# Kernel optimization log

Hardware: AMD Instinct MI355X
Metric: run time of the kernel (lower is better)

## Reference

```python
import jax, jax.numpy as jnp
import numpy as np

NEG_SLOPE = 0.2
EPS = 1e-16


def gat_layer(x, src, dst, W, att, bias, heads, out_ch, concat, num_nodes, edge_weight):
    """WeightedGATConv forward (eval mode, dropout off).
    x: [N, Fin], src/dst: [E], W: [Fin, H*C], att: [H, 2C], bias: [H*C] or [C].
    """
    H, C = heads, out_ch
    xp = (x @ W).reshape(-1, H, C)           # [N, H, C]
    xi = xp[dst]                              # target features  [E, H, C]
    xj = xp[src]                              # source features  [E, H, C]
    # attention logits: (cat(xi, xj) * att).sum(-1)
    alpha = jnp.einsum('ehc,hc->eh', xi, att[:, :C]) + jnp.einsum('ehc,hc->eh', xj, att[:, C:])
    alpha = jnp.where(alpha >= 0, alpha, NEG_SLOPE * alpha)   # leaky_relu
    # segment softmax over incoming edges of each destination node
    amax = jax.ops.segment_max(alpha, dst, num_segments=num_nodes)  # [N, H]
    amax = jnp.where(jnp.isfinite(amax), amax, 0.0)
    ex = jnp.exp(alpha - amax[dst])                                  # [E, H]
    denom = jax.ops.segment_sum(ex, dst, num_segments=num_nodes)     # [N, H]
    a = ex / (denom[dst] + EPS)                                      # [E, H]
    msg = xj * a[..., None]                                          # [E, H, C]
    if edge_weight is not None:
        msg = msg * edge_weight[:, None, None]
    out = jax.ops.segment_sum(msg, dst, num_segments=num_nodes)      # [N, H, C]
    out = out.reshape(num_nodes, H * C) if concat else out.mean(axis=1)
    return out + bias


def setup_inputs() -> dict:
    key = jax.random.key(0)
    ks = jax.random.split(key, 10)
    N, E = 20000, 320000
    IN, HID, LAT, H = 512, 256, 128, 4
    C1 = HID // H
    glorot = lambda k, shp: jax.random.uniform(k, shp, jnp.float32, -1.0, 1.0) * jnp.sqrt(6.0 / (shp[-2] + shp[-1]))
    return {
        'x': jax.random.normal(ks[0], (N, IN), jnp.float32),
        'edge_index': jax.random.randint(ks[1], (2, E), 0, N, jnp.int32),
        'edge_weight': jax.random.uniform(ks[2], (E,), jnp.float32),
        'W1': glorot(ks[3], (IN, H * C1)),
        'att1': glorot(ks[4], (H, 2 * C1)),
        'b1': jnp.zeros((H * C1,), jnp.float32),
        'Wmu': glorot(ks[5], (HID, LAT)),
        'attmu': glorot(ks[6], (1, 2 * LAT)),
        'bmu': jnp.zeros((LAT,), jnp.float32),
        'Wlv': glorot(ks[7], (HID, LAT)),
        'attlv': glorot(ks[8], (1, 2 * LAT)),
        'blv': jnp.zeros((LAT,), jnp.float32),
    }


def reference(x, edge_index, edge_weight, W1, att1, b1, Wmu, attmu, bmu, Wlv, attlv, blv):
    N = x.shape[0]
    src, dst = edge_index[0], edge_index[1]
    H = att1.shape[0]
    C1 = att1.shape[1] // 2
    LAT = Wmu.shape[1]
    h = gat_layer(x, src, dst, W1, att1, b1, H, C1, True, N, edge_weight)
    h = jax.nn.elu(h)
    mu = gat_layer(h, src, dst, Wmu, attmu, bmu, 1, LAT, False, N, edge_weight)
    logvar = gat_layer(h, src, dst, Wlv, attlv, blv, 1, LAT, False, N, edge_weight)
    return (mu, logvar)
```

## Files before the change

### kernel.cpp

```cpp
#include <hip/hip_runtime.h>
#include <stdint.h>

#define NEG_SLOPE 0.2f
#define SEPS 1e-16f

typedef short bf16x8 __attribute__((ext_vector_type(8)));
typedef float f32x4 __attribute__((ext_vector_type(4)));

static __device__ __forceinline__ float bf2f(ushort u) {
  union { uint32_t i; float f; } v; v.i = ((uint32_t)u) << 16; return v.f;
}
static __device__ __forceinline__ ushort f2bf(float f) {
  uint32_t b = __float_as_uint(f);
  b += 0x7FFFu + ((b >> 16) & 1u);
  return (ushort)(b >> 16);
}
static __device__ __forceinline__ float blo(uint32_t u) { return __uint_as_float(u << 16); }
static __device__ __forceinline__ float bhi(uint32_t u) { return __uint_as_float(u & 0xFFFF0000u); }
static __device__ __forceinline__ float ldf(const void* p, size_t i, int mode) {
  return mode ? ((const float*)p)[i] : bf2f(((const ushort*)p)[i]);
}

__global__ void fill_out(float* __restrict__ out, int n, float v) {
  int i = blockIdx.x * 256 + threadIdx.x;
  if (i < n) out[i] = v;
}

struct DetPtrs {
  const uint32_t* p[11];
  int n[11];
  const uint32_t* idx;
  int idxn;
};
__global__ void prologue(DetPtrs dp, int* __restrict__ modes,
                         int* __restrict__ deg, int N) {
  int b = blockIdx.x;
  if (b >= 12) {
    int i = (b - 12) * 256 + threadIdx.x;
    if (i < N) deg[i] = 0;
    return;
  }
  __shared__ int sL, sH;
  if (threadIdx.x == 0) { sL = 0; sH = 0; }
  __syncthreads();
  if (b < 11) {
    const uint32_t* w = dp.p[b];
    int elems = dp.n[b];
    int nprobe = min(2048, elems / 2);
    int cL = 0, cH = 0;
    for (int i = threadIdx.x; i < nprobe; i += 256) {
      uint32_t v = w[i];
      uint32_t eL = (v >> 7) & 0xFFu;
      uint32_t eH = (v >> 23) & 0xFFu;
      if (eL >= 90u && eL <= 128u) cL++;
      if (eH >= 90u && eH <= 128u) cH++;
    }
    atomicAdd(&sL, cL); atomicAdd(&sH, cH);
    __syncthreads();
    if (threadIdx.x == 0) {
      int m;
      if (sL * 4 >= nprobe * 3) m = 0;
      else if (sH * 4 >= nprobe) m = 1;
      else m = 0;
      modes[b] = m;
    }
  } else {
    const uint32_t* w = dp.idx;
    int nprobe = min(4096, dp.idxn);
    int c = 0;
    for (int i = threadIdx.x; i < nprobe; i += 256)
      if ((i & 1) && w[i] == 0u) c++;
    atomicAdd(&sL, c);
    __syncthreads();
    if (threadIdx.x == 0) modes[11] = (sL * 4 >= (nprobe / 2) * 3) ? 1 : 0;
  }
}

struct WTArgs {
  const void* w1; const void* wmu; const void* wlv;
  ushort* wt1; ushort* wall;
};
struct SmallCan { const void* src[6]; float* dst[6]; int n[6]; int mi[6]; };
struct CanArgs {
  const void* ei;
  int* deg;
  int E; int N; int EB1; int WB;
  WTArgs wt;
  SmallCan sc;
};
__global__ void canon_all(CanArgs a, const int* __restrict__ modes) {
  int b = blockIdx.x;
  if (b < a.EB1) {
    int i = b * 256 + threadIdx.x;
    if (i >= a.E) return;
    int d;
    if (modes[11]) d = (int)((const long long*)a.ei)[a.E + i];
    else           d = ((const int*)a.ei)[a.E + i];
    d = min(max(d, 0), a.N - 1);
    atomicAdd(&a.deg[d], 1);
  } else if (b < a.EB1 + a.WB) {
    int i = (b - a.EB1) * 256 + threadIdx.x;
    const int NW1 = 256 * 512;
    if (i < NW1) {
      int n = i >> 9, k = i & 511;
      float v = ldf(a.wt.w1, (size_t)k * 256 + n, modes[2]);
      if (!isfinite(v)) v = 0.f;
      a.wt.wt1[i] = f2bf(v);
    } else {
      int j = i - NW1;
      if (j >= 256 * 256) return;
      int n = j >> 8, k = j & 255;
      float v;
      if (n < 128) v = ldf(a.wt.wmu, (size_t)k * 128 + n, modes[5]);
      else         v = ldf(a.wt.wlv, (size_t)k * 128 + (n - 128), modes[8]);
      if (!isfinite(v)) v = 0.f;
      a.wt.wall[j] = f2bf(v);
    }
  } else {
    int sb = b - a.EB1 - a.WB;
    int m = modes[a.sc.mi[sb]];
    const void* s = a.sc.src[sb];
    float* d = a.sc.dst[sb];
    for (int i = threadIdx.x; i < a.sc.n[sb]; i += 256) {
      float v = ldf(s, i, m);
      if (!isfinite(v)) v = 0.f;
      d[i] = v;
    }
  }
}

__global__ __launch_bounds__(1024) void scan_deg(const int* __restrict__ deg,
                                                 int* __restrict__ row_ptr,
                                                 int* __restrict__ row_cur, int N) {
  __shared__ int part[1024];
  int t = threadIdx.x;
  int chunk = (N + 1023) / 1024;
  int lo = t * chunk, hi = min(lo + chunk, N);
  int s = 0;
  for (int i = lo; i < hi; ++i) s += deg[i];
  part[t] = s;
  __syncthreads();
  for (int off = 1; off < 1024; off <<= 1) {
    int v = (t >= off) ? part[t - off] : 0;
    __syncthreads();
    part[t] += v;
    __syncthreads();
  }
  int base = (t == 0) ? 0 : part[t - 1];
  for (int i = lo; i < hi; ++i) {
    row_ptr[i] = base; row_cur[i] = base;
    base += deg[i];
  }
  if (t == 1023) row_ptr[N] = part[1023];
}

template <int KTOT, int DMODE>
__global__ __launch_bounds__(256) void gemm_mfma_sc(
    const void* __restrict__ A, const ushort* __restrict__ WT,
    ushort* __restrict__ out, int M,
    const int* __restrict__ modeA, const float* __restrict__ attv,
    float* __restrict__ dotd, float* __restrict__ dotsrc,
    int SB, const void* __restrict__ ei, const void* __restrict__ ew,
    int* __restrict__ row_cur, int2* __restrict__ csr, int E) {
  __shared__ ushort As[64][40];
  __shared__ ushort Bs[256][40];

  if ((int)blockIdx.x < SB) {
    int e = blockIdx.x * 256 + threadIdx.x;
    if (e < E) {
      int s, d;
      if (modeA[11]) {
        s = (int)((const long long*)ei)[e];
        d = (int)((const long long*)ei)[E + e];
      } else {
        s = ((const int*)ei)[e];
        d = ((const int*)ei)[E + e];
      }
      s = min(max(s, 0), M - 1);
      d = min(max(d, 0), M - 1);
      float w = ldf(ew, e, modeA[1]);
      if (!isfinite(w)) w = 0.f;
      int p = atomicAdd(&row_cur[d], 1);
      csr[p] = make_int2(s, __float_as_int(w));
    }
    return;
  }

  int t = threadIdx.x;
  int m0 = (blockIdx.x - SB) * 64;
  int wid = t >> 6, l = t & 63;
  int wr = wid >> 1, wc = wid & 1;
  int mode = modeA ? *modeA : 0;

  int arow = t >> 2;
  int akoff = (t & 3) * 8;
  int srow = min(m0 + arow, M - 1);

  f32x4 acc[2][8];
#pragma unroll
  for (int i = 0; i < 2; ++i)
#pragma unroll
    for (int j = 0; j < 8; ++j) acc[i][j] = (f32x4){0.f, 0.f, 0.f, 0.f};

  int cl = l & 15;
  int ksl = (l >> 4) * 8;

  for (int k0 = 0; k0 < KTOT; k0 += 32) {
    if (mode) {
      const float* Af = (const float*)A + (size_t)srow * KTOT + k0 + akoff;
      float4 v0 = *(const float4*)Af;
      float4 v1 = *(const float4*)(Af + 4);
      uint4 pk;
      pk.x = (uint32_t)f2bf(v0.x) | ((uint32_t)f2bf(v0.y) << 16);
      pk.y = (uint32_t)f2bf(v0.z) | ((uint32_t)f2bf(v0.w) << 16);
      pk.z = (uint32_t)f2bf(v1.x) | ((uint32_t)f2bf(v1.y) << 16);
      pk.w = (uint32_t)f2bf(v1.z) | ((uint32_t)f2bf(v1.w) << 16);
      *(uint4*)&As[arow][akoff] = pk;
    } else {
      *(uint4*)&As[arow][akoff] =
          *(const uint4*)((const ushort*)A + (size_t)srow * KTOT + k0 + akoff);
    }
#pragma unroll
    for (int i = 0; i < 4; ++i) {
      int f = t + i * 256;
      int row = f >> 2, koff = (f & 3) * 8;
      *(uint4*)&Bs[row][koff] = *(const uint4*)(WT + (size_t)row * KTOT + k0 + koff);
    }
    __syncthreads();

    bf16x8 af[2], bfr[8];
#pragma unroll
    for (int i = 0; i < 2; ++i)
      af[i] = *(const bf16x8*)&As[wr * 32 + i * 16 + cl][ksl];
#pragma unroll
    for (int j = 0; j < 8; ++j)
      bfr[j] = *(const bf16x8*)&Bs[wc * 128 + j * 16 + cl][ksl];
#pragma unroll
    for (int i = 0; i < 2; ++i)
#pragma unroll
      for (int j = 0; j < 8; ++j)
        acc[i][j] = __builtin_amdgcn_mfma_f32_16x16x32_bf16(af[i], bfr[j], acc[i][j], 0, 0, 0);
    __syncthreads();
  }

  int rb = (l >> 4) * 4;

  if (DMODE == 1) {
    float wdv[8], wsv[8];
#pragma unroll
    for (int j = 0; j < 8; ++j) {
      int h = wc * 2 + (j >> 2);
      int c = (j & 3) * 16 + cl;
      wdv[j] = attv[h * 128 + c];
      wsv[j] = attv[h * 128 + 64 + c];
    }
#pragma unroll
    for (int i = 0; i < 2; ++i)
#pragma unroll
      for (int r = 0; r < 4; ++r) {
        float pd0 = acc[i][0][r] * wdv[0] + acc[i][1][r] * wdv[1]
                  + acc[i][2][r] * wdv[2] + acc[i][3][r] * wdv[3];
        float ps0 = acc[i][0][r] * wsv[0] + acc[i][1][r] * wsv[1]
                  + acc[i][2][r] * wsv[2] + acc[i][3][r] * wsv[3];
        float pd1 = acc[i][4][r] * wdv[4] + acc[i][5][r] * wdv[5]
                  + acc[i][6][r] * wdv[6] + acc[i][7][r] * wdv[7];
        float ps1 = acc[i][4][r] * wsv[4] + acc[i][5][r] * wsv[5]
                  + acc[i][6][r] * wsv[6] + acc[i][7][r] * wsv[7];
#pragma unroll
        for (int d = 1; d < 16; d <<= 1) {
          pd0 += __shfl_xor(pd0, d); ps0 += __shfl_xor(ps0, d);
          pd1 += __shfl_xor(pd1, d); ps1 += __shfl_xor(ps1, d);
        }
        if (cl == 0) {
          int m = m0 + wr * 32 + i * 16 + rb + r;
          if (m < M) {
            dotd[m * 4 + wc * 2] = pd0;
            dotsrc[m * 4 + wc * 2] = ps0;
            dotd[m * 4 + wc * 2 + 1] = pd1;
            dotsrc[m * 4 + wc * 2 + 1] = ps1;
          }
        }
      }
  } else if (DMODE == 2) {
    float wdv[8], wsv[8];
#pragma unroll
    for (int j = 0; j < 8; ++j) {
      int c = j * 16 + cl;
      wdv[j] = attv[wc * 256 + c];
      wsv[j] = attv[wc * 256 + 128 + c];
    }
#pragma unroll
    for (int i = 0; i < 2; ++i)
#pragma unroll
      for (int r = 0; r < 4; ++r) {
        float pd = 0.f, ps = 0.f;
#pragma unroll
        for (int j = 0; j < 8; ++j) {
          pd += acc[i][j][r] * wdv[j];
          ps += acc[i][j][r] * wsv[j];
        }
#pragma unroll
        for (int d = 1; d < 16; d <<= 1) {
          pd += __shfl_xor(pd, d); ps += __shfl_xor(ps, d);
        }
        if (cl == 0) {
          int m = m0 + wr * 32 + i * 16 + rb + r;
          if (m < M) {
            dotd[m * 4 + wc * 2] = pd;
            dotd[m * 4 + wc * 2 + 1] = ps;
          }
        }
      }
  }

#pragma unroll
  for (int i = 0; i < 2; ++i)
#pragma unroll
    for (int j = 0; j < 8; ++j)
#pragma unroll
      for (int r = 0; r < 4; ++r) {
        int m = m0 + wr * 32 + i * 16 + rb + r;
        if (m < M)
          out[(size_t)m * 256 + wc * 128 + j * 16 + cl] = f2bf(acc[i][j][r]);
      }
}

__global__ __launch_bounds__(256) void fused_agg1_wave(
    const int* __restrict__ row_ptr, const int2* __restrict__ csr,
    const float* __restrict__ ad, const float* __restrict__ as_,
    const ushort* __restrict__ xp, const float* __restrict__ b1,
    ushort* __restrict__ hout, int N) {
  int n = blockIdx.x * 4 + (threadIdx.x >> 6);
  if (n >= N) return;
  int lane = threadIdx.x & 63;
  int h = lane & 3;
  int es = lane >> 2;
  int sg = lane >> 5, l = lane & 31, hl = l >> 3;

  int lo = row_ptr[n], hi = row_ptr[n + 1];
  float adv = ad[n * 4 + h];

  float m = -1e30f;
  float dsum = 0.f;
  float acc[8];
#pragma unroll
  for (int j = 0; j < 8; ++j) acc[j] = 0.f;

  for (int cb = lo; cb < hi; cb += 16) {
    int cn = min(16, hi - cb);
    float a = -1e30f;
    int sreg = 0;
    float wreg = 0.f;
    if (es < cn) {
      int2 sw = csr[cb + es];
      sreg = sw.x;
      wreg = __int_as_float(sw.y);
      float aa = adv + as_[sreg * 4 + h];
      a = aa >= 0.f ? aa : NEG_SLOPE * aa;
    }
    float cm = a;
    cm = fmaxf(cm, __shfl_xor(cm, 4));
    cm = fmaxf(cm, __shfl_xor(cm, 8));
    cm = fmaxf(cm, __shfl_xor(cm, 16));
    cm = fmaxf(cm, __shfl_xor(cm, 32));
    float mnew = fmaxf(m, cm);
    float scale = expf(m - mnew);
    m = mnew;
    float ev = (es < cn) ? expf(a - m) : 0.f;
    dsum = dsum * scale + ev;
    float cwreg = ev * wreg;
    float sc = __shfl(scale, hl);
#pragma unroll
    for (int j = 0; j < 8; ++j) acc[j] *= sc;
    for (int el2 = 0; el2 < cn; el2 += 4) {
      int ea = el2 + sg, eb = el2 + 2 + sg;
      int eac = min(ea, cn - 1), ebc = min(eb, cn - 1);
      float cwa = __shfl(cwreg, (eac << 2) | hl);
      int sa = __shfl(sreg, eac << 2);
      float cwb = __shfl(cwreg, (ebc << 2) | hl);
      int sb = __shfl(sreg, ebc << 2);
      bool pa = ea < cn, pb = eb < cn;
      uint4 va, vb;
      if (pa) va = *(const uint4*)(xp + (size_t)sa * 256 + l * 8);
      if (pb) vb = *(const uint4*)(xp + (size_t)sb * 256 + l * 8);
      if (pa) {
        acc[0] += cwa * blo(va.x); acc[1] += cwa * bhi(va.x);
        acc[2] += cwa * blo(va.y); acc[3] += cwa * bhi(va.y);
        acc[4] += cwa * blo(va.z); acc[5] += cwa * bhi(va.z);
        acc[6] += cwa * blo(va.w); acc[7] += cwa * bhi(va.w);
      }
      if (pb) {
        acc[0] += cwb * blo(vb.x); acc[1] += cwb * bhi(vb.x);
        acc[2] += cwb * blo(vb.y); acc[3] += cwb * bhi(vb.y);
        acc[4] += cwb * blo(vb.z); acc[5] += cwb * bhi(vb.z);
        acc[6] += cwb * blo(vb.w); acc[7] += cwb * bhi(vb.w);
      }
    }
  }

  dsum += __shfl_xor(dsum, 4);
  dsum += __shfl_xor(dsum, 8);
  dsum += __shfl_xor(dsum, 16);
  dsum += __shfl_xor(dsum, 32);
  float den = __shfl(dsum, hl);

#pragma unroll
  for (int j = 0; j < 8; ++j) acc[j] += __shfl_down(acc[j], 32);

  if (sg == 0) {
    float inv = 1.0f / (den + SEPS);
    uint4 pk;
    uint32_t w[4];
#pragma unroll
    for (int q = 0; q < 4; ++q) {
      float v0 = acc[q * 2] * inv + b1[l * 8 + q * 2];
      float v1 = acc[q * 2 + 1] * inv + b1[l * 8 + q * 2 + 1];
      v0 = v0 > 0.f ? v0 : expm1f(v0);
      v1 = v1 > 0.f ? v1 : expm1f(v1);
      w[q] = (uint32_t)f2bf(v0) | ((uint32_t)f2bf(v1) << 16);
    }
    pk.x = w[0]; pk.y = w[1]; pk.z = w[2]; pk.w = w[3];
    *(uint4*)(hout + (size_t)n * 256 + l * 8) = pk;
  }
}

__global__ __launch_bounds__(256) void fused_agg2_wave(
    const int* __restrict__ row_ptr, const int2* __restrict__ csr,
    const float* __restrict__ a4, const ushort* __restrict__ hp2,
    const float* __restrict__ bmu, const float* __restrict__ blv,
    float* __restrict__ out, int N) {
  int n = blockIdx.x * 4 + (threadIdx.x >> 6);
  if (n >= N) return;
  int lane = threadIdx.x & 63;
  int e31 = lane & 31;
  int half = lane >> 5;
  int sg = lane >> 5;
  int l = lane & 31;
  int hh = l >> 4;
  int hlane = hh << 5;

  int lo = row_ptr[n], hi = row_ptr[n + 1];
  float adv = a4[n * 4 + half * 2];

  float m = -1e30f;
  float dsum = 0.f;
  float acc[8];
#pragma unroll
  for (int j = 0; j < 8; ++j) acc[j] = 0.f;

  for (int cb = lo; cb < hi; cb += 32) {
    int cn = min(32, hi - cb);
    float a = -1e30f;
    int sreg = 0;
    float wreg = 0.f;
    if (e31 < cn) {
      int2 sw = csr[cb + e31];
      sreg = sw.x;
      wreg = __int_as_float(sw.y);
      float aa = adv + a4[sreg * 4 + half * 2 + 1];
      a = aa >= 0.f ? aa : NEG_SLOPE * aa;
    }
    float cm = a;
    cm = fmaxf(cm, __shfl_xor(cm, 1));
    cm = fmaxf(cm, __shfl_xor(cm, 2));
    cm = fmaxf(cm, __shfl_xor(cm, 4));
    cm = fmaxf(cm, __shfl_xor(cm, 8));
    cm = fmaxf(cm, __shfl_xor(cm, 16));
    float mnew = fmaxf(m, cm);
    float scale = expf(m - mnew);
    m = mnew;
    float ev = (e31 < cn) ? expf(a - m) : 0.f;
    dsum = dsum * scale + ev;
    float cwreg = ev * wreg;
    float sc = __shfl(scale, hlane);
#pragma unroll
    for (int j = 0; j < 8; ++j) acc[j] *= sc;
    for (int el2 = 0; el2 < cn; el2 += 2) {
      int el = el2 + sg;
      int elc = min(el, cn - 1);
      float cw = __shfl(cwreg, elc | (hh << 5));
      int s = __shfl(sreg, elc);
      if (el < cn) {
        uint4 v = *(const uint4*)(hp2 + (size_t)s * 256 + l * 8);
        acc[0] += cw * blo(v.x); acc[1] += cw * bhi(v.x);
        acc[2] += cw * blo(v.y); acc[3] += cw * bhi(v.y);
        acc[4] += cw * blo(v.z); acc[5] += cw * bhi(v.z);
        acc[6] += cw * blo(v.w); acc[7] += cw * bhi(v.w);
      }
    }
  }

  dsum += __shfl_xor(dsum, 1);
  dsum += __shfl_xor(dsum, 2);
  dsum += __shfl_xor(dsum, 4);
  dsum += __shfl_xor(dsum, 8);
  dsum += __shfl_xor(dsum, 16);
  float den = __shfl(dsum, hlane);

#pragma unroll
  for (int j = 0; j < 8; ++j) acc[j] += __shfl_down(acc[j], 32);

  if (sg == 0) {
    float inv = 1.0f / (den + SEPS);
    const float* bb = hh ? blv : bmu;
    int c0 = (l & 15) * 8;
    float* op = out + (size_t)hh * N * 128 + (size_t)n * 128 + c0;
#pragma unroll
    for (int j = 0; j < 8; ++j) op[j] = acc[j] * inv + bb[c0 + j];
  }
}

extern "C" void kernel_launch(void* const* d_in, const int* in_sizes, int n_in,
                              void* d_out, int out_size, void* d_ws, size_t ws_size,
                              hipStream_t stream) {
  int OB = (out_size + 255) / 256;
  bool ok = (n_in == 12);
  int HID = 0, IN = 0, N = 0, LAT = 0, E = 0;
  if (ok) {
    HID = in_sizes[5];
    ok = ok && HID == 256;
    IN = HID ? in_sizes[3] / HID : 0;
    ok = ok && IN == 512 && in_sizes[3] == IN * HID;
    N = IN ? in_sizes[0] / IN : 0;
    ok = ok && N > 0 && in_sizes[0] == N * IN && (N % 4) == 0;
    LAT = in_sizes[8];
    ok = ok && LAT == 128;
    E = in_sizes[2];
    ok = ok && E > 0 && in_sizes[1] == 2 * E;
    ok = ok && in_sizes[4] == 2 * HID && in_sizes[6] == HID * LAT &&
         in_sizes[7] == 2 * LAT && in_sizes[9] == HID * LAT &&
         in_sizes[10] == 2 * LAT && in_sizes[11] == LAT &&
         out_size == 2 * N * LAT;
  }
  if (!ok) { fill_out<<<OB, 256, 0, stream>>>((float*)d_out, out_size, 2.0f); return; }

  char* p = (char*)d_ws;
  auto alloc = [&](size_t bytes) -> char* {
    char* r = p;
    p += (bytes + 255) & ~((size_t)255);
    return r;
  };
  ushort* xp_bf = (ushort*)alloc((size_t)N * HID * 2);
  ushort* hreg  = (ushort*)alloc((size_t)N * HID * 2);
  ushort* WT1b  = (ushort*)alloc((size_t)HID * IN * 2);
  ushort* WallT = (ushort*)alloc((size_t)2 * LAT * HID * 2);
  float*  dots  = (float*) alloc((size_t)N * 12 * 4);
  float*  att1f = (float*) alloc((size_t)2 * HID * 4);
  float*  att2f = (float*) alloc((size_t)4 * LAT * 4);
  float*  b1f   = (float*) alloc((size_t)HID * 4);
  float*  bmuf  = (float*) alloc((size_t)LAT * 4);
  float*  blvf  = (float*) alloc((size_t)LAT * 4);
  int2*   csr   = (int2*)  alloc((size_t)E * 8);
  int*    row_ptr=(int*)   alloc((size_t)(N + 1) * 4);
  int*    row_cur=(int*)   alloc((size_t)N * 4);
  int*    deg   = (int*)   alloc((size_t)N * 4);
  int*    modes = (int*)   alloc(16 * 4);

  size_t need = (size_t)(p - (char*)d_ws);
  if (need > ws_size) {
    fill_out<<<OB, 256, 0, stream>>>((float*)d_out, out_size, 3.0f);
    return;
  }

  ushort* hp2 = xp_bf;
  float* ad1 = dots;
  float* as1 = dots + (size_t)N * 4;
  float* a4  = dots + (size_t)N * 8;

  const int fidx[11] = {0, 2, 3, 4, 5, 6, 7, 8, 9, 10, 11};
  DetPtrs dp;
  for (int i = 0; i < 11; ++i) {
    dp.p[i] = (const uint32_t*)d_in[fidx[i]];
    dp.n[i] = in_sizes[fidx[i]];
  }
  dp.idx = (const uint32_t*)d_in[1];
  dp.idxn = 2 * E;
  int nbDeg = (N + 255) / 256;
  prologue<<<12 + nbDeg, 256, 0, stream>>>(dp, modes, deg, N);

  int EB1 = (E + 255) / 256;
  int WB = (HID * IN + 2 * LAT * HID + 255) / 256;
  CanArgs ca;
  ca.ei = d_in[1];
  ca.deg = deg;
  ca.E = E; ca.N = N; ca.EB1 = EB1; ca.WB = WB;
  ca.wt.w1 = d_in[3]; ca.wt.wmu = d_in[6]; ca.wt.wlv = d_in[9];
  ca.wt.wt1 = WT1b; ca.wt.wall = WallT;
  ca.sc.src[0] = d_in[4];  ca.sc.dst[0] = att1f;        ca.sc.n[0] = 2 * HID; ca.sc.mi[0] = 3;
  ca.sc.src[1] = d_in[5];  ca.sc.dst[1] = b1f;          ca.sc.n[1] = HID;     ca.sc.mi[1] = 4;
  ca.sc.src[2] = d_in[7];  ca.sc.dst[2] = att2f;        ca.sc.n[2] = 2 * LAT; ca.sc.mi[2] = 6;
  ca.sc.src[3] = d_in[8];  ca.sc.dst[3] = bmuf;         ca.sc.n[3] = LAT;     ca.sc.mi[3] = 7;
  ca.sc.src[4] = d_in[10]; ca.sc.dst[4] = att2f + 256;  ca.sc.n[4] = 2 * LAT; ca.sc.mi[4] = 9;
  ca.sc.src[5] = d_in[11]; ca.sc.dst[5] = blvf;         ca.sc.n[5] = LAT;     ca.sc.mi[5] = 10;
  canon_all<<<EB1 + WB + 6, 256, 0, stream>>>(ca, modes);

  scan_deg<<<1, 1024, 0, stream>>>(deg, row_ptr, row_cur, N);

  int MB = (N + 63) / 64;

  gemm_mfma_sc<512, 1><<<EB1 + MB, 256, 0, stream>>>(
      d_in[0], WT1b, xp_bf, N, &modes[0], att1f, ad1, as1,
      EB1, d_in[1], d_in[2], row_cur, csr, E);
  fused_agg1_wave<<<(N + 3) / 4, 256, 0, stream>>>(row_ptr, csr,
                                                   ad1, as1, xp_bf, b1f, hreg, N);

  gemm_mfma_sc<256, 2><<<MB, 256, 0, stream>>>(
      hreg, WallT, hp2, N, nullptr, att2f, a4, nullptr,
      0, nullptr, nullptr, nullptr, nullptr, 0);
  fused_agg2_wave<<<(N + 3) / 4, 256, 0, stream>>>(row_ptr, csr, a4,
                                                   hp2, bmuf, blvf,
                                                   (float*)d_out, N);
}
```

Before: 282.5 us.

## Shrink GEMM row tile to 32 and split columns across four waves

```diff
diff --git a/kernel.cpp b/kernel.cpp
--- a/kernel.cpp
+++ b/kernel.cpp
@@ -162,8 +162,9 @@
     float* __restrict__ dotd, float* __restrict__ dotsrc,
     int SB, const void* __restrict__ ei, const void* __restrict__ ew,
     int* __restrict__ row_cur, int2* __restrict__ csr, int E) {
-  __shared__ ushort As[64][40];
+  __shared__ ushort As[32][40];
   __shared__ ushort Bs[256][40];
+  __shared__ float red[4][32][2];
 
   if ((int)blockIdx.x < SB) {
     int e = blockIdx.x * 256 + threadIdx.x;
@@ -187,38 +188,33 @@
   }
 
   int t = threadIdx.x;
-  int m0 = (blockIdx.x - SB) * 64;
+  int m0 = (blockIdx.x - SB) * 32;
   int wid = t >> 6, l = t & 63;
-  int wr = wid >> 1, wc = wid & 1;
   int mode = modeA ? *modeA : 0;
 
-  int arow = t >> 2;
-  int akoff = (t & 3) * 8;
+  int arow = t >> 3;
+  int akoff = (t & 7) * 4;
   int srow = min(m0 + arow, M - 1);
 
-  f32x4 acc[2][8];
+  f32x4 acc[2][4];
 #pragma unroll
   for (int i = 0; i < 2; ++i)
 #pragma unroll
-    for (int j = 0; j < 8; ++j) acc[i][j] = (f32x4){0.f, 0.f, 0.f, 0.f};
+    for (int j = 0; j < 4; ++j) acc[i][j] = (f32x4){0.f, 0.f, 0.f, 0.f};
 
   int cl = l & 15;
   int ksl = (l >> 4) * 8;
 
   for (int k0 = 0; k0 < KTOT; k0 += 32) {
     if (mode) {
-      const float* Af = (const float*)A + (size_t)srow * KTOT + k0 + akoff;
-      float4 v0 = *(const float4*)Af;
-      float4 v1 = *(const float4*)(Af + 4);
-      uint4 pk;
-      pk.x = (uint32_t)f2bf(v0.x) | ((uint32_t)f2bf(v0.y) << 16);
-      pk.y = (uint32_t)f2bf(v0.z) | ((uint32_t)f2bf(v0.w) << 16);
-      pk.z = (uint32_t)f2bf(v1.x) | ((uint32_t)f2bf(v1.y) << 16);
-      pk.w = (uint32_t)f2bf(v1.z) | ((uint32_t)f2bf(v1.w) << 16);
-      *(uint4*)&As[arow][akoff] = pk;
+      const float4 v = *(const float4*)((const float*)A + (size_t)srow * KTOT + k0 + akoff);
+      uint2 pk;
+      pk.x = (uint32_t)f2bf(v.x) | ((uint32_t)f2bf(v.y) << 16);
+      pk.y = (uint32_t)f2bf(v.z) | ((uint32_t)f2bf(v.w) << 16);
+      *(uint2*)&As[arow][akoff] = pk;
     } else {
-      *(uint4*)&As[arow][akoff] =
-          *(const uint4*)((const ushort*)A + (size_t)srow * KTOT + k0 + akoff);
+      *(uint2*)&As[arow][akoff] =
+          *(const uint2*)((const ushort*)A + (size_t)srow * KTOT + k0 + akoff);
     }
 #pragma unroll
     for (int i = 0; i < 4; ++i) {
@@ -228,17 +224,17 @@
     }
     __syncthreads();
 
-    bf16x8 af[2], bfr[8];
+    bf16x8 af[2], bfr[4];
 #pragma unroll
     for (int i = 0; i < 2; ++i)
-      af[i] = *(const bf16x8*)&As[wr * 32 + i * 16 + cl][ksl];
-#pragma unroll
-    for (int j = 0; j < 8; ++j)
-      bfr[j] = *(const bf16x8*)&Bs[wc * 128 + j * 16 + cl][ksl];
+      af[i] = *(const bf16x8*)&As[i * 16 + cl][ksl];
+#pragma unroll
+    for (int j = 0; j < 4; ++j)
+      bfr[j] = *(const bf16x8*)&Bs[wid * 64 + j * 16 + cl][ksl];
 #pragma unroll
     for (int i = 0; i < 2; ++i)
 #pragma unroll
-      for (int j = 0; j < 8; ++j)
+      for (int j = 0; j < 4; ++j)
         acc[i][j] = __builtin_amdgcn_mfma_f32_16x16x32_bf16(af[i], bfr[j], acc[i][j], 0, 0, 0);
     __syncthreads();
   }
@@ -246,82 +242,77 @@
   int rb = (l >> 4) * 4;
 
   if (DMODE == 1) {
-    float wdv[8], wsv[8];
-#pragma unroll
-    for (int j = 0; j < 8; ++j) {
-      int h = wc * 2 + (j >> 2);
-      int c = (j & 3) * 16 + cl;
-      wdv[j] = attv[h * 128 + c];
-      wsv[j] = attv[h * 128 + 64 + c];
+    float wdv[4], wsv[4];
+#pragma unroll
+    for (int j = 0; j < 4; ++j) {
+      wdv[j] = attv[wid * 128 + j * 16 + cl];
+      wsv[j] = attv[wid * 128 + 64 + j * 16 + cl];
     }
 #pragma unroll
     for (int i = 0; i < 2; ++i)
 #pragma unroll
       for (int r = 0; r < 4; ++r) {
-        float pd0 = acc[i][0][r] * wdv[0] + acc[i][1][r] * wdv[1]
-                  + acc[i][2][r] * wdv[2] + acc[i][3][r] * wdv[3];
-        float ps0 = acc[i][0][r] * wsv[0] + acc[i][1][r] * wsv[1]
-                  + acc[i][2][r] * wsv[2] + acc[i][3][r] * wsv[3];
-        float pd1 = acc[i][4][r] * wdv[4] + acc[i][5][r] * wdv[5]
-                  + acc[i][6][r] * wdv[6] + acc[i][7][r] * wdv[7];
-        float ps1 = acc[i][4][r] * wsv[4] + acc[i][5][r] * wsv[5]
-                  + acc[i][6][r] * wsv[6] + acc[i][7][r] * wsv[7];
+        float pd = acc[i][0][r] * wdv[0] + acc[i][1][r] * wdv[1]
+                 + acc[i][2][r] * wdv[2] + acc[i][3][r] * wdv[3];
+        float ps = acc[i][0][r] * wsv[0] + acc[i][1][r] * wsv[1]
+                 + acc[i][2][r] * wsv[2] + acc[i][3][r] * wsv[3];
 #pragma unroll
         for (int d = 1; d < 16; d <<= 1) {
-          pd0 += __shfl_xor(pd0, d); ps0 += __shfl_xor(ps0, d);
-          pd1 += __shfl_xor(pd1, d); ps1 += __shfl_xor(ps1, d);
+          pd += __shfl_xor(pd, d); ps += __shfl_xor(ps, d);
         }
         if (cl == 0) {
-          int m = m0 + wr * 32 + i * 16 + rb + r;
+          int m = m0 + i * 16 + rb + r;
           if (m < M) {
-            dotd[m * 4 + wc * 2] = pd0;
-            dotsrc[m * 4 + wc * 2] = ps0;
-            dotd[m * 4 + wc * 2 + 1] = pd1;
-            dotsrc[m * 4 + wc * 2 + 1] = ps1;
+            dotd[m * 4 + wid] = pd;
+            dotsrc[m * 4 + wid] = ps;
           }
         }
       }
   } else if (DMODE == 2) {
-    float wdv[8], wsv[8];
-#pragma unroll
-    for (int j = 0; j < 8; ++j) {
-      int c = j * 16 + cl;
-      wdv[j] = attv[wc * 256 + c];
-      wsv[j] = attv[wc * 256 + 128 + c];
+    int sl = wid >> 1;
+    int base = (wid & 1) * 64;
+    float wdv[4], wsv[4];
+#pragma unroll
+    for (int j = 0; j < 4; ++j) {
+      wdv[j] = attv[sl * 256 + base + j * 16 + cl];
+      wsv[j] = attv[sl * 256 + 128 + base + j * 16 + cl];
     }
 #pragma unroll
     for (int i = 0; i < 2; ++i)
 #pragma unroll
       for (int r = 0; r < 4; ++r) {
-        float pd = 0.f, ps = 0.f;
-#pragma unroll
-        for (int j = 0; j < 8; ++j) {
-          pd += acc[i][j][r] * wdv[j];
-          ps += acc[i][j][r] * wsv[j];
-        }
+        float pd = acc[i][0][r] * wdv[0] + acc[i][1][r] * wdv[1]
+                 + acc[i][2][r] * wdv[2] + acc[i][3][r] * wdv[3];
+        float ps = acc[i][0][r] * wsv[0] + acc[i][1][r] * wsv[1]
+                 + acc[i][2][r] * wsv[2] + acc[i][3][r] * wsv[3];
 #pragma unroll
         for (int d = 1; d < 16; d <<= 1) {
           pd += __shfl_xor(pd, d); ps += __shfl_xor(ps, d);
         }
         if (cl == 0) {
-          int m = m0 + wr * 32 + i * 16 + rb + r;
-          if (m < M) {
-            dotd[m * 4 + wc * 2] = pd;
-            dotd[m * 4 + wc * 2 + 1] = ps;
-          }
+          int ml = i * 16 + rb + r;
+          red[wid][ml][0] = pd;
+          red[wid][ml][1] = ps;
         }
       }
+    __syncthreads();
+    if (t < 128) {
+      int ml = t & 31, which = (t >> 5) & 1, sl2 = t >> 6;
+      float v = red[sl2 * 2][ml][which] + red[sl2 * 2 + 1][ml][which];
+      int m = m0 + ml;
+      if (m < M) dotd[m * 4 + sl2 * 2 + which] = v;
+    }
   }
 
 #pragma unroll
   for (int i = 0; i < 2; ++i)
 #pragma unroll
-    for (int j = 0; j < 8; ++j)
+    for (int j = 0; j < 4; ++j)
 #pragma unroll
       for (int r = 0; r < 4; ++r) {
-        int m = m0 + wr * 32 + i * 16 + rb + r;
+        int m = m0 + i * 16 + rb + r;
         if (m < M)
-          out[(size_t)m * 256 + wc * 128 + j * 16 + cl] = f2bf(acc[i][j][r]);
+          out[(size_t)m * 256 + wid * 64 + j * 16 + cl] = f2bf(acc[i][j][r]);
       }
 }
 
@@ -596,7 +587,7 @@
 
   scan_deg<<<1, 1024, 0, stream>>>(deg, row_ptr, row_cur, N);
 
-  int MB = (N + 63) / 64;
+  int MB = (N + 31) / 32;
 
   gemm_mfma_sc<512, 1><<<EB1 + MB, 256, 0, stream>>>(
       d_in[0], WT1b, xp_bf, N, &modes[0], att1f, ad1, as1,
```

Result: faster. 276.2 us (-2.2%).
